# Optimization experiments

Hardware: AMD Instinct MI355X
Metric: run time of the kernel (lower is better)

The kernel has to match this reference:

```python
import jax, jax.numpy as jnp
import numpy as np

N_NODES = 50000
N_EDGES = 800000
IN_F = 512
OUT_F = 96
ALPHA = 0.1
ITERATIONS = 10
AVG_DEG = 16


def setup_inputs() -> dict:
    key = jax.random.key(0)
    k1, k2, k3, k4, k5 = jax.random.split(key, 5)
    x = jax.random.normal(k1, (N_NODES, IN_F), dtype=jnp.float32)
    # xavier_uniform with gain=1.414 over [IN_F, OUT_F]
    limit = 1.414 * np.sqrt(6.0 / (IN_F + OUT_F))
    weight = jax.random.uniform(k2, (IN_F, OUT_F), dtype=jnp.float32,
                                minval=-limit, maxval=limit)
    edge_src = jax.random.randint(k3, (N_EDGES,), 0, N_NODES, dtype=jnp.int32)
    edge_dst = jax.random.randint(k4, (N_EDGES,), 0, N_NODES, dtype=jnp.int32)
    # values scaled like a row-normalized adjacency for stable propagation
    edge_val = jax.random.uniform(k5, (N_EDGES,), dtype=jnp.float32) / AVG_DEG
    return {"x": x, "weight": weight, "edge_src": edge_src,
            "edge_dst": edge_dst, "edge_val": edge_val}


def _spmm(edge_src, edge_dst, edge_val, h):
    # out[i] = sum_{edges e with dst=i} val[e] * h[src[e]]
    gathered = h[edge_src] * edge_val[:, None]          # [E, OUT_F]
    return jax.ops.segment_sum(gathered, edge_dst, num_segments=N_NODES)


def reference(x, weight, edge_src, edge_dst, edge_val):
    support = x @ weight                                 # [N, OUT_F]
    prev = support
    def body(_, s):
        s = _spmm(edge_src, edge_dst, edge_val, s) * (1.0 - ALPHA) + prev * ALPHA
        return jax.nn.relu(s)
    return jax.lax.fori_loop(0, ITERATIONS, body, support)
```

## Files before the change

kernel.cpp:

```cpp
#include <hip/hip_runtime.h>

typedef unsigned int   uint;
typedef unsigned short ushort;
typedef __attribute__((ext_vector_type(8))) short bf16x8;
typedef __attribute__((ext_vector_type(4))) float f32x4;

#define N_NODES 50000
#define N_EDGES 800000
#define IN_F    512
#define OUT_F   96
#define SCAN_BLOCKS 196
#define TPN 12

__device__ __forceinline__ float bflo(uint u) { return __uint_as_float(u << 16); }
__device__ __forceinline__ float bfhi(uint u) { return __uint_as_float(u & 0xffff0000u); }
__device__ __forceinline__ uint f2bf(float x) {
    uint u = __float_as_uint(x);
    return (u + 0x7fffu + ((u >> 16) & 1u)) >> 16;
}
__device__ __forceinline__ uint pack2bf(float lo, float hi) {
    return f2bf(lo) | (f2bf(hi) << 16);
}

__global__ __launch_bounds__(256) void wt_kernel(const float* __restrict__ w,
                                                 ushort* __restrict__ wT) {
    int t = blockIdx.x * 256 + threadIdx.x;
    if (t < IN_F * OUT_F) {
        int k = t / OUT_F, c = t - k * OUT_F;
        wT[(size_t)c * IN_F + k] = (ushort)f2bf(w[t]);
    }
}

__global__ __launch_bounds__(256) void gemm_kernel(const float* __restrict__ x,
                                                   const ushort* __restrict__ wT,
                                                   ushort* __restrict__ supB) {
    const int tid  = threadIdx.x;
    const int wv   = tid >> 6;
    const int lane = tid & 63;
    const int m    = lane & 15;
    const int quad = lane >> 4;

    const int row  = blockIdx.x * 64 + wv * 16 + m;
    const int arow = (row < N_NODES) ? row : (N_NODES - 1);
    const float* xp = x + (size_t)arow * IN_F + quad * 8;

    f32x4 acc[6];
    #pragma unroll
    for (int ct = 0; ct < 6; ++ct) acc[ct] = (f32x4){0.f, 0.f, 0.f, 0.f};

    for (int k0 = 0; k0 < IN_F; k0 += 32) {
        float4 xa = *(const float4*)(xp + k0);
        float4 xb = *(const float4*)(xp + k0 + 4);
        union { uint u[4]; bf16x8 v; } af;
        af.u[0] = pack2bf(xa.x, xa.y); af.u[1] = pack2bf(xa.z, xa.w);
        af.u[2] = pack2bf(xb.x, xb.y); af.u[3] = pack2bf(xb.z, xb.w);
        #pragma unroll
        for (int ct = 0; ct < 6; ++ct) {
            bf16x8 bf = *(const bf16x8*)(wT + (size_t)(ct * 16 + m) * IN_F
                                            + k0 + quad * 8);
            acc[ct] = __builtin_amdgcn_mfma_f32_16x16x32_bf16(af.v, bf, acc[ct],
                                                              0, 0, 0);
        }
    }

    const int orow0 = blockIdx.x * 64 + wv * 16 + quad * 4;
    #pragma unroll
    for (int ct = 0; ct < 6; ++ct) {
        #pragma unroll
        for (int r = 0; r < 4; ++r) {
            int gr = orow0 + r;
            if (gr < N_NODES)
                supB[(size_t)gr * OUT_F + ct * 16 + m] = (ushort)f2bf(acc[ct][r]);
        }
    }
}

__global__ void zero_kernel(int* __restrict__ p, int n) {
    int t = blockIdx.x * blockDim.x + threadIdx.x;
    if (t < n) p[t] = 0;
}

__global__ void hist_kernel(const int* __restrict__ dst, int* __restrict__ counts) {
    int e = blockIdx.x * blockDim.x + threadIdx.x;
    if (e < N_EDGES) atomicAdd(&counts[dst[e]], 1);
}

__global__ __launch_bounds__(256) void block_reduce_kernel(const int* __restrict__ counts,
                                                           int* __restrict__ blockSums) {
    __shared__ int s[256];
    int idx = blockIdx.x * 256 + threadIdx.x;
    s[threadIdx.x] = (idx < N_NODES) ? counts[idx] : 0;
    __syncthreads();
    for (int off = 128; off > 0; off >>= 1) {
        if (threadIdx.x < off) s[threadIdx.x] += s[threadIdx.x + off];
        __syncthreads();
    }
    if (threadIdx.x == 0) blockSums[blockIdx.x] = s[0];
}

__global__ __launch_bounds__(256) void scan_sums_kernel(int* __restrict__ blockSums,
                                                        int* __restrict__ blockOffs,
                                                        int* __restrict__ rowstart) {
    __shared__ int s[256];
    int t = threadIdx.x;
    s[t] = (t < SCAN_BLOCKS) ? blockSums[t] : 0;
    __syncthreads();
    for (int off = 1; off < 256; off <<= 1) {
        int v = (t >= off) ? s[t - off] : 0;
        __syncthreads();
        s[t] += v;
        __syncthreads();
    }
    if (t < SCAN_BLOCKS) blockOffs[t] = (t == 0) ? 0 : s[t - 1];
    if (t == 0) rowstart[N_NODES] = s[SCAN_BLOCKS - 1];
}

__global__ __launch_bounds__(256) void block_scan_kernel(const int* __restrict__ counts,
                                                         const int* __restrict__ blockOffs,
                                                         int* __restrict__ rowstart,
                                                         int* __restrict__ cursor) {
    __shared__ int s[256];
    int t   = threadIdx.x;
    int idx = blockIdx.x * 256 + t;
    int v   = (idx < N_NODES) ? counts[idx] : 0;
    s[t] = v;
    __syncthreads();
    for (int off = 1; off < 256; off <<= 1) {
        int u = (t >= off) ? s[t - off] : 0;
        __syncthreads();
        s[t] += u;
        __syncthreads();
    }
    if (idx < N_NODES) {
        int excl = blockOffs[blockIdx.x] + s[t] - v;
        rowstart[idx] = excl;
        cursor[idx]   = excl;
    }
}

__global__ void scatter_kernel(const int* __restrict__ src, const int* __restrict__ dst,
                               const float* __restrict__ val, int* __restrict__ cursor,
                               int2* __restrict__ edgeP) {
    int e = blockIdx.x * blockDim.x + threadIdx.x;
    if (e < N_EDGES) {
        int d   = dst[e];
        int pos = atomicAdd(&cursor[d], 1);
        edgeP[pos] = make_int2(src[e], __float_as_int(val[e]));
    }
}

__device__ __forceinline__ void acc8(float* a, float v, uint4 hv) {
    a[0] = fmaf(v, bflo(hv.x), a[0]); a[1] = fmaf(v, bfhi(hv.x), a[1]);
    a[2] = fmaf(v, bflo(hv.y), a[2]); a[3] = fmaf(v, bfhi(hv.y), a[3]);
    a[4] = fmaf(v, bflo(hv.z), a[4]); a[5] = fmaf(v, bfhi(hv.z), a[5]);
    a[6] = fmaf(v, bflo(hv.w), a[6]); a[7] = fmaf(v, bfhi(hv.w), a[7]);
}

template <bool FINAL>
__global__ __launch_bounds__(256) void prop_kernel(const ushort* __restrict__ h,
                                                   const ushort* __restrict__ sup,
                                                   const int* __restrict__ rowstart,
                                                   const int2* __restrict__ edgeP,
                                                   ushort* __restrict__ outB,
                                                   float* __restrict__ outF) {
    int t = blockIdx.x * 256 + threadIdx.x;
    int i = t / TPN;
    if (i >= N_NODES) return;
    int q = t - i * TPN;
    int f = q * 8;

    int start = rowstart[i];
    int end   = rowstart[i + 1];

    float a[8] = {0.f, 0.f, 0.f, 0.f, 0.f, 0.f, 0.f, 0.f};
    int e = start;
    for (; e + 3 < end; e += 4) {
        int2 e0 = edgeP[e];
        int2 e1 = edgeP[e + 1];
        int2 e2 = edgeP[e + 2];
        int2 e3 = edgeP[e + 3];
        uint4 h0 = *(const uint4*)(h + (size_t)e0.x * OUT_F + f);
        uint4 h1 = *(const uint4*)(h + (size_t)e1.x * OUT_F + f);
        uint4 h2 = *(const uint4*)(h + (size_t)e2.x * OUT_F + f);
        uint4 h3 = *(const uint4*)(h + (size_t)e3.x * OUT_F + f);
        acc8(a, __int_as_float(e0.y), h0);
        acc8(a, __int_as_float(e1.y), h1);
        acc8(a, __int_as_float(e2.y), h2);
        acc8(a, __int_as_float(e3.y), h3);
    }
    for (; e < end; ++e) {
        int2 e0 = edgeP[e];
        uint4 h0 = *(const uint4*)(h + (size_t)e0.x * OUT_F + f);
        acc8(a, __int_as_float(e0.y), h0);
    }

    size_t o = (size_t)i * OUT_F + f;
    uint4 sp = *(const uint4*)(sup + o);
    float r[8];
    r[0] = fmaxf(fmaf(a[0], 0.9f, bflo(sp.x) * 0.1f), 0.f);
    r[1] = fmaxf(fmaf(a[1], 0.9f, bfhi(sp.x) * 0.1f), 0.f);
    r[2] = fmaxf(fmaf(a[2], 0.9f, bflo(sp.y) * 0.1f), 0.f);
    r[3] = fmaxf(fmaf(a[3], 0.9f, bfhi(sp.y) * 0.1f), 0.f);
    r[4] = fmaxf(fmaf(a[4], 0.9f, bflo(sp.z) * 0.1f), 0.f);
    r[5] = fmaxf(fmaf(a[5], 0.9f, bfhi(sp.z) * 0.1f), 0.f);
    r[6] = fmaxf(fmaf(a[6], 0.9f, bflo(sp.w) * 0.1f), 0.f);
    r[7] = fmaxf(fmaf(a[7], 0.9f, bfhi(sp.w) * 0.1f), 0.f);

    if (FINAL) {
        *(float4*)(outF + o)     = make_float4(r[0], r[1], r[2], r[3]);
        *(float4*)(outF + o + 4) = make_float4(r[4], r[5], r[6], r[7]);
    } else {
        *(uint4*)(outB + o) = make_uint4(pack2bf(r[0], r[1]), pack2bf(r[2], r[3]),
                                         pack2bf(r[4], r[5]), pack2bf(r[6], r[7]));
    }
}

extern "C" void kernel_launch(void* const* d_in, const int* in_sizes, int n_in,
                              void* d_out, int out_size, void* d_ws, size_t ws_size,
                              hipStream_t stream) {
    const float* x    = (const float*)d_in[0];
    const float* w    = (const float*)d_in[1];
    const int*   esrc = (const int*)d_in[2];
    const int*   edst = (const int*)d_in[3];
    const float* eval = (const float*)d_in[4];
    float* out = (float*)d_out;

    const size_t supBytes = (size_t)N_NODES * OUT_F * sizeof(ushort);
    ushort* supB = (ushort*)d_out;
    ushort* wTb  = (ushort*)((char*)d_out + (size_t)out_size * 4
                             - (size_t)IN_F * OUT_F * sizeof(ushort));

    char*  xb  = (char*)d_in[0];
    size_t off = 0;
    auto alloc = [&](size_t bytes) -> char* {
        char* p = xb + off;
        off = (off + bytes + 255) & ~(size_t)255;
        return p;
    };
    ushort* supB2     = (ushort*)alloc(supBytes);
    ushort* hU        = (ushort*)alloc(supBytes);
    ushort* hV        = (ushort*)alloc(supBytes);
    int2*   edgeP     = (int2*)alloc((size_t)N_EDGES * sizeof(int2));
    int*    rowstart  = (int*)alloc((N_NODES + 1) * sizeof(int));
    int*    cursor    = (int*)alloc(N_NODES * sizeof(int));
    int*    counts    = (int*)alloc(N_NODES * sizeof(int));
    int*    blockSums = (int*)alloc(SCAN_BLOCKS * sizeof(int));
    int*    blockOffs = (int*)alloc(SCAN_BLOCKS * sizeof(int));

    wt_kernel<<<(IN_F * OUT_F + 255) / 256, 256, 0, stream>>>(w, wTb);

    gemm_kernel<<<(N_NODES + 63) / 64, 256, 0, stream>>>(x, wTb, supB);

    hipMemcpyAsync(supB2, supB, supBytes, hipMemcpyDeviceToDevice, stream);

    zero_kernel<<<(N_NODES + 255) / 256, 256, 0, stream>>>(counts, N_NODES);
    hist_kernel<<<(N_EDGES + 255) / 256, 256, 0, stream>>>(edst, counts);
    block_reduce_kernel<<<SCAN_BLOCKS, 256, 0, stream>>>(counts, blockSums);
    scan_sums_kernel<<<1, 256, 0, stream>>>(blockSums, blockOffs, rowstart);
    block_scan_kernel<<<SCAN_BLOCKS, 256, 0, stream>>>(counts, blockOffs,
                                                       rowstart, cursor);
    scatter_kernel<<<(N_EDGES + 255) / 256, 256, 0, stream>>>(esrc, edst, eval,
                                                              cursor, edgeP);

    const int pgrid = (N_NODES * TPN + 255) / 256;
    const ushort* in = supB2;
    for (int it = 1; it <= 9; ++it) {
        ushort* o = (it & 1) ? hU : hV;
        prop_kernel<false><<<pgrid, 256, 0, stream>>>(in, supB2, rowstart, edgeP,
                                                      o, nullptr);
        in = o;
    }
    prop_kernel<true><<<pgrid, 256, 0, stream>>>(in, supB2, rowstart, edgeP,
                                                 nullptr, out);
}
```

Before: 562.3 us.

## Reorder nodes by in-degree bins, prefetch GEMM operands, unroll SpMM by eight

Nodes are relabelled by a counting sort on in-degree, so that neighbouring threads in the propagation kernel handle rows of similar length and wavefront divergence drops. The CSR, the support matrix and the source indices are built in the permuted order, and the final output is scattered back through the permutation. The GEMM now double-buffers its x and weight loads in registers, and the SpMM inner loop issues eight gathers at a time instead of four for more memory-level parallelism. In exchange there are several extra small preprocessing kernels, and the permuted support copy replaces the old memcpy.

```diff
diff --git a/kernel.cpp b/kernel.cpp
--- a/kernel.cpp
+++ b/kernel.cpp
@@ -11,6 +11,7 @@
 #define OUT_F   96
 #define SCAN_BLOCKS 196
 #define TPN 12
+#define NBINS 64
 
 __device__ __forceinline__ float bflo(uint u) { return __uint_as_float(u << 16); }
 __device__ __forceinline__ float bfhi(uint u) { return __uint_as_float(u & 0xffff0000u); }
@@ -42,25 +43,48 @@
 
     const int row  = blockIdx.x * 64 + wv * 16 + m;
     const int arow = (row < N_NODES) ? row : (N_NODES - 1);
-    const float* xp = x + (size_t)arow * IN_F + quad * 8;
+    const float*  xp = x  + (size_t)arow * IN_F + quad * 8;
+    const ushort* wp = wT + (size_t)m * IN_F + quad * 8;
 
     f32x4 acc[6];
     #pragma unroll
     for (int ct = 0; ct < 6; ++ct) acc[ct] = (f32x4){0.f, 0.f, 0.f, 0.f};
 
-    for (int k0 = 0; k0 < IN_F; k0 += 32) {
-        float4 xa = *(const float4*)(xp + k0);
-        float4 xb = *(const float4*)(xp + k0 + 4);
+    float4 xa = *(const float4*)(xp);
+    float4 xb = *(const float4*)(xp + 4);
+    bf16x8 b[6];
+    #pragma unroll
+    for (int ct = 0; ct < 6; ++ct)
+        b[ct] = *(const bf16x8*)(wp + (size_t)ct * 16 * IN_F);
+
+    #pragma unroll
+    for (int it = 0; it < 15; ++it) {
+        const int kn = (it + 1) * 32;
+        float4 xa2 = *(const float4*)(xp + kn);
+        float4 xb2 = *(const float4*)(xp + kn + 4);
+        bf16x8 b2[6];
+        #pragma unroll
+        for (int ct = 0; ct < 6; ++ct)
+            b2[ct] = *(const bf16x8*)(wp + (size_t)ct * 16 * IN_F + kn);
         union { uint u[4]; bf16x8 v; } af;
         af.u[0] = pack2bf(xa.x, xa.y); af.u[1] = pack2bf(xa.z, xa.w);
         af.u[2] = pack2bf(xb.x, xb.y); af.u[3] = pack2bf(xb.z, xb.w);
         #pragma unroll
-        for (int ct = 0; ct < 6; ++ct) {
-            bf16x8 bf = *(const bf16x8*)(wT + (size_t)(ct * 16 + m) * IN_F
-                                            + k0 + quad * 8);
-            acc[ct] = __builtin_amdgcn_mfma_f32_16x16x32_bf16(af.v, bf, acc[ct],
-                                                              0, 0, 0);
-        }
+        for (int ct = 0; ct < 6; ++ct)
+            acc[ct] = __builtin_amdgcn_mfma_f32_16x16x32_bf16(af.v, b[ct],
+                                                              acc[ct], 0, 0, 0);
+        xa = xa2; xb = xb2;
+        #pragma unroll
+        for (int ct = 0; ct < 6; ++ct) b[ct] = b2[ct];
+    }
+    {
+        union { uint u[4]; bf16x8 v; } af;
+        af.u[0] = pack2bf(xa.x, xa.y); af.u[1] = pack2bf(xa.z, xa.w);
+        af.u[2] = pack2bf(xb.x, xb.y); af.u[3] = pack2bf(xb.z, xb.w);
+        #pragma unroll
+        for (int ct = 0; ct < 6; ++ct)
+            acc[ct] = __builtin_amdgcn_mfma_f32_16x16x32_bf16(af.v, b[ct],
+                                                              acc[ct], 0, 0, 0);
     }
 
     const int orow0 = blockIdx.x * 64 + wv * 16 + quad * 4;
@@ -85,11 +109,48 @@
     if (e < N_EDGES) atomicAdd(&counts[dst[e]], 1);
 }
 
+__global__ void degbin_kernel(const int* __restrict__ counts, int* __restrict__ bins) {
+    int n = blockIdx.x * blockDim.x + threadIdx.x;
+    if (n < N_NODES) {
+        int b = counts[n]; if (b > NBINS - 1) b = NBINS - 1;
+        atomicAdd(&bins[b], 1);
+    }
+}
+
+__global__ __launch_bounds__(64) void binscan_kernel(const int* __restrict__ bins,
+                                                     int* __restrict__ binCur) {
+    __shared__ int s[NBINS];
+    int t = threadIdx.x;
+    s[t] = bins[t];
+    __syncthreads();
+    for (int off = 1; off < NBINS; off <<= 1) {
+        int v = (t >= off) ? s[t - off] : 0;
+        __syncthreads();
+        s[t] += v;
+        __syncthreads();
+    }
+    binCur[t] = s[t] - bins[t];
+}
+
+__global__ void permscatter_kernel(const int* __restrict__ counts,
+                                   int* __restrict__ binCur,
+                                   int* __restrict__ perm,
+                                   int* __restrict__ invperm) {
+    int n = blockIdx.x * blockDim.x + threadIdx.x;
+    if (n < N_NODES) {
+        int b = counts[n]; if (b > NBINS - 1) b = NBINS - 1;
+        int pos = atomicAdd(&binCur[b], 1);
+        perm[pos]  = n;
+        invperm[n] = pos;
+    }
+}
+
 __global__ __launch_bounds__(256) void block_reduce_kernel(const int* __restrict__ counts,
+                                                           const int* __restrict__ perm,
                                                            int* __restrict__ blockSums) {
     __shared__ int s[256];
     int idx = blockIdx.x * 256 + threadIdx.x;
-    s[threadIdx.x] = (idx < N_NODES) ? counts[idx] : 0;
+    s[threadIdx.x] = (idx < N_NODES) ? counts[perm[idx]] : 0;
     __syncthreads();
     for (int off = 128; off > 0; off >>= 1) {
         if (threadIdx.x < off) s[threadIdx.x] += s[threadIdx.x + off];
@@ -116,13 +177,14 @@
 }
 
 __global__ __launch_bounds__(256) void block_scan_kernel(const int* __restrict__ counts,
+                                                         const int* __restrict__ perm,
                                                          const int* __restrict__ blockOffs,
                                                          int* __restrict__ rowstart,
                                                          int* __restrict__ cursor) {
     __shared__ int s[256];
     int t   = threadIdx.x;
     int idx = blockIdx.x * 256 + t;
-    int v   = (idx < N_NODES) ? counts[idx] : 0;
+    int v   = (idx < N_NODES) ? counts[perm[idx]] : 0;
     s[t] = v;
     __syncthreads();
     for (int off = 1; off < 256; off <<= 1) {
@@ -139,14 +201,26 @@
 }
 
 __global__ void scatter_kernel(const int* __restrict__ src, const int* __restrict__ dst,
-                               const float* __restrict__ val, int* __restrict__ cursor,
-                               int2* __restrict__ edgeP) {
+                               const float* __restrict__ val,
+                               const int* __restrict__ invperm,
+                               int* __restrict__ cursor, int2* __restrict__ edgeP) {
     int e = blockIdx.x * blockDim.x + threadIdx.x;
     if (e < N_EDGES) {
-        int d   = dst[e];
-        int pos = atomicAdd(&cursor[d], 1);
-        edgeP[pos] = make_int2(src[e], __float_as_int(val[e]));
-    }
+        int dnew = invperm[dst[e]];
+        int pos  = atomicAdd(&cursor[dnew], 1);
+        edgeP[pos] = make_int2(invperm[src[e]], __float_as_int(val[e]));
+    }
+}
+
+__global__ void permsup_kernel(const ushort* __restrict__ supB,
+                               const int* __restrict__ perm,
+                               ushort* __restrict__ supP) {
+    int t = blockIdx.x * blockDim.x + threadIdx.x;
+    int j = t / TPN;
+    if (j >= N_NODES) return;
+    int q = t - j * TPN;
+    *(uint4*)(supP + (size_t)j * OUT_F + q * 8) =
+        *(const uint4*)(supB + (size_t)perm[j] * OUT_F + q * 8);
 }
 
 __device__ __forceinline__ void acc8(float* a, float v, uint4 hv) {
@@ -161,6 +235,7 @@
                                                    const ushort* __restrict__ sup,
                                                    const int* __restrict__ rowstart,
                                                    const int2* __restrict__ edgeP,
+                                                   const int* __restrict__ perm,
                                                    ushort* __restrict__ outB,
                                                    float* __restrict__ outF) {
     int t = blockIdx.x * 256 + threadIdx.x;
@@ -174,19 +249,16 @@
 
     float a[8] = {0.f, 0.f, 0.f, 0.f, 0.f, 0.f, 0.f, 0.f};
     int e = start;
-    for (; e + 3 < end; e += 4) {
-        int2 e0 = edgeP[e];
-        int2 e1 = edgeP[e + 1];
-        int2 e2 = edgeP[e + 2];
-        int2 e3 = edgeP[e + 3];
-        uint4 h0 = *(const uint4*)(h + (size_t)e0.x * OUT_F + f);
-        uint4 h1 = *(const uint4*)(h + (size_t)e1.x * OUT_F + f);
-        uint4 h2 = *(const uint4*)(h + (size_t)e2.x * OUT_F + f);
-        uint4 h3 = *(const uint4*)(h + (size_t)e3.x * OUT_F + f);
-        acc8(a, __int_as_float(e0.y), h0);
-        acc8(a, __int_as_float(e1.y), h1);
-        acc8(a, __int_as_float(e2.y), h2);
-        acc8(a, __int_as_float(e3.y), h3);
+    for (; e + 7 < end; e += 8) {
+        int2 ed[8];
+        #pragma unroll
+        for (int u = 0; u < 8; ++u) ed[u] = edgeP[e + u];
+        uint4 hv[8];
+        #pragma unroll
+        for (int u = 0; u < 8; ++u)
+            hv[u] = *(const uint4*)(h + (size_t)ed[u].x * OUT_F + f);
+        #pragma unroll
+        for (int u = 0; u < 8; ++u) acc8(a, __int_as_float(ed[u].y), hv[u]);
     }
     for (; e < end; ++e) {
         int2 e0 = edgeP[e];
@@ -207,8 +279,9 @@
     r[7] = fmaxf(fmaf(a[7], 0.9f, bfhi(sp.w) * 0.1f), 0.f);
 
     if (FINAL) {
-        *(float4*)(outF + o)     = make_float4(r[0], r[1], r[2], r[3]);
-        *(float4*)(outF + o + 4) = make_float4(r[4], r[5], r[6], r[7]);
+        size_t oo = (size_t)perm[i] * OUT_F + f;
+        *(float4*)(outF + oo)     = make_float4(r[0], r[1], r[2], r[3]);
+        *(float4*)(outF + oo + 4) = make_float4(r[4], r[5], r[6], r[7]);
     } else {
         *(uint4*)(outB + o) = make_uint4(pack2bf(r[0], r[1]), pack2bf(r[2], r[3]),
                                          pack2bf(r[4], r[5]), pack2bf(r[6], r[7]));
@@ -237,39 +310,48 @@
         off = (off + bytes + 255) & ~(size_t)255;
         return p;
     };
-    ushort* supB2     = (ushort*)alloc(supBytes);
+    ushort* supP      = (ushort*)alloc(supBytes);
     ushort* hU        = (ushort*)alloc(supBytes);
     ushort* hV        = (ushort*)alloc(supBytes);
     int2*   edgeP     = (int2*)alloc((size_t)N_EDGES * sizeof(int2));
     int*    rowstart  = (int*)alloc((N_NODES + 1) * sizeof(int));
     int*    cursor    = (int*)alloc(N_NODES * sizeof(int));
     int*    counts    = (int*)alloc(N_NODES * sizeof(int));
+    int*    perm      = (int*)alloc(N_NODES * sizeof(int));
+    int*    invperm   = (int*)alloc(N_NODES * sizeof(int));
+    int*    binsAll   = (int*)alloc(2 * NBINS * sizeof(int));
     int*    blockSums = (int*)alloc(SCAN_BLOCKS * sizeof(int));
     int*    blockOffs = (int*)alloc(SCAN_BLOCKS * sizeof(int));
+    int* bins   = binsAll;
+    int* binCur = binsAll + NBINS;
 
     wt_kernel<<<(IN_F * OUT_F + 255) / 256, 256, 0, stream>>>(w, wTb);
 
     gemm_kernel<<<(N_NODES + 63) / 64, 256, 0, stream>>>(x, wTb, supB);
 
-    hipMemcpyAsync(supB2, supB, supBytes, hipMemcpyDeviceToDevice, stream);
-
     zero_kernel<<<(N_NODES + 255) / 256, 256, 0, stream>>>(counts, N_NODES);
+    zero_kernel<<<1, 2 * NBINS, 0, stream>>>(binsAll, 2 * NBINS);
     hist_kernel<<<(N_EDGES + 255) / 256, 256, 0, stream>>>(edst, counts);
-    block_reduce_kernel<<<SCAN_BLOCKS, 256, 0, stream>>>(counts, blockSums);
+    degbin_kernel<<<(N_NODES + 255) / 256, 256, 0, stream>>>(counts, bins);
+    binscan_kernel<<<1, NBINS, 0, stream>>>(bins, binCur);
+    permscatter_kernel<<<(N_NODES + 255) / 256, 256, 0, stream>>>(counts, binCur,
+                                                                  perm, invperm);
+    block_reduce_kernel<<<SCAN_BLOCKS, 256, 0, stream>>>(counts, perm, blockSums);
     scan_sums_kernel<<<1, 256, 0, stream>>>(blockSums, blockOffs, rowstart);
-    block_scan_kernel<<<SCAN_BLOCKS, 256, 0, stream>>>(counts, blockOffs,
+    block_scan_kernel<<<SCAN_BLOCKS, 256, 0, stream>>>(counts, perm, blockOffs,
                                                        rowstart, cursor);
     scatter_kernel<<<(N_EDGES + 255) / 256, 256, 0, stream>>>(esrc, edst, eval,
-                                                              cursor, edgeP);
+                                                              invperm, cursor, edgeP);
+    permsup_kernel<<<(N_NODES * TPN + 255) / 256, 256, 0, stream>>>(supB, perm, supP);
 
     const int pgrid = (N_NODES * TPN + 255) / 256;
-    const ushort* in = supB2;
+    const ushort* in = supP;
     for (int it = 1; it <= 9; ++it) {
         ushort* o = (it & 1) ? hU : hV;
-        prop_kernel<false><<<pgrid, 256, 0, stream>>>(in, supB2, rowstart, edgeP,
-                                                      o, nullptr);
+        prop_kernel<false><<<pgrid, 256, 0, stream>>>(in, supP, rowstart, edgeP,
+                                                      perm, o, nullptr);
         in = o;
     }
-    prop_kernel<true><<<pgrid, 256, 0, stream>>>(in, supB2, rowstart, edgeP,
-                                                 nullptr, out);
-}
+    prop_kernel<true><<<pgrid, 256, 0, stream>>>(in, supP, rowstart, edgeP,
+                                                 perm, nullptr, out);
+}
```

New measurement: 843.7 us. 50.0% more time.
